# Kernel optimization log

Measured on AMD Instinct MI355X. Metric: run time of the kernel, lower is better.

Reference implementation:

```python
import jax, jax.numpy as jnp
import numpy as np


def _gcn_conv(x, edge_index, W, b):
    # PyG GCNConv: h = D^{-1/2} (A + I) D^{-1/2} (x @ W) + b
    n = x.shape[0]
    xw = x @ W  # [N, C]
    loop = jnp.arange(n, dtype=edge_index.dtype)
    row = jnp.concatenate([edge_index[0], loop])  # source (x_j)
    col = jnp.concatenate([edge_index[1], loop])  # target (aggregation index)
    deg = jax.ops.segment_sum(jnp.ones_like(col, dtype=xw.dtype), col, num_segments=n)
    dinv = jnp.where(deg > 0, deg ** -0.5, 0.0)
    norm = dinv[row] * dinv[col]  # [E+N]
    out = jax.ops.segment_sum(xw[row] * norm[:, None], col, num_segments=n)
    return out + b


def setup_inputs() -> dict:
    key = jax.random.key(0)
    ks = jax.random.split(key, 8)
    N, F, E = 100000, 512, 3200000
    W_SCALE = 0.1  # keep sigmoid un-saturated
    x = jax.random.normal(ks[0], (N, F), dtype=jnp.float32)
    edge_index = jax.random.randint(ks[1], (2, E), 0, N, dtype=jnp.int64)
    Wg = jax.random.normal(ks[2], (F, 16), dtype=jnp.float32) * W_SCALE
    bg = jnp.zeros((16,), dtype=jnp.float32)
    W1 = jax.random.normal(ks[3], (16, 16), dtype=jnp.float32) * W_SCALE
    b1 = jnp.zeros((16,), dtype=jnp.float32)
    W2 = jax.random.normal(ks[4], (16, 32), dtype=jnp.float32) * W_SCALE
    b2 = jnp.zeros((32,), dtype=jnp.float32)
    W3 = jax.random.normal(ks[5], (32, 1), dtype=jnp.float32) * W_SCALE
    b3 = jnp.zeros((1,), dtype=jnp.float32)
    return {"x": x, "edge_index": edge_index, "Wg": Wg, "bg": bg,
            "W1": W1, "b1": b1, "W2": W2, "b2": b2, "W3": W3, "b3": b3}


def reference(x, edge_index, Wg, bg, W1, b1, W2, b2, W3, b3):
    h = jax.nn.relu(_gcn_conv(x, edge_index, Wg, bg))
    h = jax.nn.relu(h @ W1 + b1)
    h = jax.nn.relu(h @ W2 + b2)
    return jax.nn.sigmoid(h @ W3 + b3)  # [N, 1]
```

## Files before the change

### kernel.cpp

```cpp
#include <hip/hip_runtime.h>
#include <math.h>


static constexpr int F = 512;
static constexpr int C = 16;
static constexpr int BSH = 7;
static constexpr int BSZ = 128;
static constexpr int NBMAX = 1024;
static constexpr int EPB = 16384;

__global__ __launch_bounds__(256) void k_xw_bcount(const float* __restrict__ x,
                                                   const float* __restrict__ Wg,
                                                   float* __restrict__ xw, int n,
                                                   const int* __restrict__ dst,
                                                   int* __restrict__ bh, int E, int gb)
{
    if ((int)blockIdx.x >= gb) {
        __shared__ int hist[NBMAX];
        for (int i = threadIdx.x; i < NBMAX; i += 256) hist[i] = 0;
        __syncthreads();
        int g = blockIdx.x - gb;
        int base = g * EPB;
#pragma unroll 4
        for (int j = 0; j < EPB / 256; ++j) {
            int e = base + j * 256 + threadIdx.x;
            if (e < E) atomicAdd(&hist[dst[e] >> BSH], 1);
        }
        __syncthreads();
        int* row = bh + (size_t)g * NBMAX;
        for (int i = threadIdx.x; i < NBMAX; i += 256) row[i] = hist[i];
        return;
    }
    int row = blockIdx.x * 256 + threadIdx.x;
    if (row >= n) return;
    float acc[C];
#pragma unroll
    for (int c = 0; c < C; ++c) acc[c] = 0.f;
    const float4* xr = (const float4*)(x + (size_t)row * F);
#pragma unroll 8
    for (int k4 = 0; k4 < F / 4; ++k4) {
        float4 xv = xr[k4];
        const float* w = Wg + k4 * 4 * C;
#pragma unroll
        for (int j = 0; j < 4; ++j) {
            float xs = (j == 0) ? xv.x : (j == 1) ? xv.y : (j == 2) ? xv.z : xv.w;
#pragma unroll
            for (int c = 0; c < C; ++c)
                acc[c] = fmaf(xs, w[j * C + c], acc[c]);
        }
    }
    float4* o = (float4*)(xw + (size_t)row * C);
#pragma unroll
    for (int q = 0; q < 4; ++q)
        o[q] = make_float4(acc[4 * q + 0], acc[4 * q + 1], acc[4 * q + 2], acc[4 * q + 3]);
}

__global__ __launch_bounds__(256) void k_bscatter(const int* __restrict__ ei,
                                                  const int* __restrict__ bh,
                                                  int* __restrict__ bstart,
                                                  int* __restrict__ packed,
                                                  int E, int geb)
{
    __shared__ int s_excl[NBMAX];
    __shared__ int cur[NBMAX];
    int g = blockIdx.x, t = threadIdx.x;

    int own[4], tot[4];
#pragma unroll
    for (int k = 0; k < 4; ++k) { own[k] = 0; tot[k] = 0; }
    int gg = 0;
    for (; gg + 4 <= geb; gg += 4) {
        int v[4][4];
#pragma unroll
        for (int j = 0; j < 4; ++j)
#pragma unroll
            for (int k = 0; k < 4; ++k)
                v[j][k] = bh[(size_t)(gg + j) * NBMAX + t + 256 * k];
#pragma unroll
        for (int j = 0; j < 4; ++j)
#pragma unroll
            for (int k = 0; k < 4; ++k) {
                if (gg + j == g) own[k] = tot[k];
                tot[k] += v[j][k];
            }
    }
    for (; gg < geb; ++gg) {
#pragma unroll
        for (int k = 0; k < 4; ++k) {
            int v = bh[(size_t)gg * NBMAX + t + 256 * k];
            if (gg == g) own[k] = tot[k];
            tot[k] += v;
        }
    }
#pragma unroll
    for (int k = 0; k < 4; ++k) s_excl[t + 256 * k] = tot[k];
    __syncthreads();

    int c0 = s_excl[4 * t], c1 = s_excl[4 * t + 1],
        c2 = s_excl[4 * t + 2], c3 = s_excl[4 * t + 3];
    int csum = c0 + c1 + c2 + c3;
    cur[t] = csum;
    __syncthreads();
    for (int d = 1; d < 256; d <<= 1) {
        int u = (t >= d) ? cur[t - d] : 0;
        __syncthreads();
        cur[t] += u;
        __syncthreads();
    }
    int chunk_excl = cur[t] - csum;
    __syncthreads();

    int e0 = chunk_excl, e1 = e0 + c0, e2 = e1 + c1, e3 = e2 + c2;
    s_excl[4 * t] = e0; s_excl[4 * t + 1] = e1;
    s_excl[4 * t + 2] = e2; s_excl[4 * t + 3] = e3;
    __syncthreads();

#pragma unroll
    for (int k = 0; k < 4; ++k)
        cur[t + 256 * k] = s_excl[t + 256 * k] + own[k];
    if (g == 0) {
#pragma unroll
        for (int k = 0; k < 4; ++k) bstart[t + 256 * k] = s_excl[t + 256 * k];
        if (t == 255) bstart[NBMAX] = e3 + c3;
    }
    __syncthreads();

    int base = g * EPB;
#pragma unroll 2
    for (int j = 0; j < EPB / 256; ++j) {
        int e = base + j * 256 + t;
        if (e < E) {
            int d = ei[E + e];
            int s = ei[e];
            int b = d >> BSH;
            int r = atomicAdd(&cur[b], 1);
            packed[r] = s | ((d & (BSZ - 1)) << 17);
        }
    }
}

__global__ __launch_bounds__(256) void k_bcsr(const int* __restrict__ packed,
                                              const int* __restrict__ bstart,
                                              float* __restrict__ y,
                                              int* __restrict__ srcs,
                                              int* __restrict__ starts,
                                              int* __restrict__ cnt,
                                              float* __restrict__ dinv, int n)
{
    int b = blockIdx.x, t = threadIdx.x;
    __shared__ int hist[BSZ];
    __shared__ int sc[BSZ];
    __shared__ float sdi[BSZ];
    if (t < BSZ) hist[t] = 0;
    __syncthreads();
    int beg = bstart[b], end = bstart[b + 1];
    for (int e = beg + t; e < end; e += 256)
        atomicAdd(&hist[(packed[e] >> 17) & (BSZ - 1)], 1);
    __syncthreads();
    int myc = 0;
    if (t < BSZ) { myc = hist[t]; sc[t] = myc; }
    __syncthreads();
    for (int d = 1; d < BSZ; d <<= 1) {
        int u = 0;
        if (t < BSZ && t >= d) u = sc[t - d];
        __syncthreads();
        if (t < BSZ) sc[t] += u;
        __syncthreads();
    }
    int node0 = b << BSH;
    if (t < BSZ) {
        int lst = sc[t] - myc;
        sc[t] = lst;
        float di = rsqrtf((float)(myc + 1));
        sdi[t] = di;
        int node = node0 + t;
        if (node < n) { starts[node] = beg + lst; cnt[node] = myc; dinv[node] = di; }
        hist[t] = 0;
    }
    __syncthreads();
    for (int e = beg + t; e < end; e += 256) {
        int p = packed[e];
        int dl = (p >> 17) & (BSZ - 1);
        int r = atomicAdd(&hist[dl], 1);
        srcs[beg + sc[dl] + r] = p & 0x1FFFF;
    }
    int nn = n - node0; if (nn > BSZ) nn = BSZ;
    if (nn <= 0) return;
    int lim = nn * 4;
    float4* yv = (float4*)(y + (size_t)node0 * C);
    for (int i = t; i < lim; i += 256) {
        float di = sdi[i >> 2];
        float4 v = yv[i];
        v.x *= di; v.y *= di; v.z *= di; v.w *= di;
        yv[i] = v;
    }
}

__global__ __launch_bounds__(256) void k_gather_mlp(const float* __restrict__ y,
                                                    const int* __restrict__ srcs,
                                                    const int* __restrict__ starts,
                                                    const int* __restrict__ cnt,
                                                    const float* __restrict__ dinv,
                                                    const float* __restrict__ bg,
                                                    const float* __restrict__ W1,
                                                    const float* __restrict__ b1,
                                                    const float* __restrict__ W2,
                                                    const float* __restrict__ b2,
                                                    const float* __restrict__ W3,
                                                    const float* __restrict__ b3,
                                                    float* __restrict__ out, int n)
{
    __shared__ float sh[64][17];
    int tid = threadIdx.x;
    int gtid = blockIdx.x * 256 + tid;
    int i = gtid >> 2;
    int q = tid & 3;
    if (i < n) {
        const float4* yv = (const float4*)y;
        float4 acc = yv[(size_t)i * 4 + q];
        int beg = starts[i];
        int end = beg + cnt[i];
        int e = beg;
        int headEnd = (beg + 3) & ~3;
        if (headEnd > end) headEnd = end;
        for (; e < headEnd; ++e) {
            float4 v = yv[(size_t)srcs[e] * 4 + q];
            acc.x += v.x; acc.y += v.y; acc.z += v.z; acc.w += v.w;
        }
        for (; e + 4 <= end; e += 4) {
            int4 s4 = *(const int4*)(srcs + e);
            float4 v0 = yv[(size_t)s4.x * 4 + q];
            float4 v1 = yv[(size_t)s4.y * 4 + q];
            float4 v2 = yv[(size_t)s4.z * 4 + q];
            float4 v3 = yv[(size_t)s4.w * 4 + q];
            acc.x += v0.x + v1.x + v2.x + v3.x;
            acc.y += v0.y + v1.y + v2.y + v3.y;
            acc.z += v0.z + v1.z + v2.z + v3.z;
            acc.w += v0.w + v1.w + v2.w + v3.w;
        }
        for (; e < end; ++e) {
            float4 v = yv[(size_t)srcs[e] * 4 + q];
            acc.x += v.x; acc.y += v.y; acc.z += v.z; acc.w += v.w;
        }
        float di = dinv[i];
        const float* bq = bg + q * 4;
        int lr = tid >> 2;
        sh[lr][4 * q + 0] = fmaxf(fmaf(acc.x, di, bq[0]), 0.f);
        sh[lr][4 * q + 1] = fmaxf(fmaf(acc.y, di, bq[1]), 0.f);
        sh[lr][4 * q + 2] = fmaxf(fmaf(acc.z, di, bq[2]), 0.f);
        sh[lr][4 * q + 3] = fmaxf(fmaf(acc.w, di, bq[3]), 0.f);
    }
    __syncthreads();
    if (tid < 64) {
        int node = blockIdx.x * 64 + tid;
        if (node < n) {
            float h[16];
#pragma unroll
            for (int k = 0; k < 16; ++k) h[k] = sh[tid][k];
            float h1[16];
#pragma unroll
            for (int c = 0; c < 16; ++c) {
                float s = b1[c];
#pragma unroll
                for (int k = 0; k < 16; ++k) s = fmaf(h[k], W1[k * 16 + c], s);
                h1[c] = fmaxf(s, 0.f);
            }
            float h2[32];
#pragma unroll
            for (int c = 0; c < 32; ++c) {
                float s = b2[c];
#pragma unroll
                for (int k = 0; k < 16; ++k) s = fmaf(h1[k], W2[k * 32 + c], s);
                h2[c] = fmaxf(s, 0.f);
            }
            float s = b3[0];
#pragma unroll
            for (int k = 0; k < 32; ++k) s = fmaf(h2[k], W3[k], s);
            out[node] = 1.f / (1.f + expf(-s));
        }
    }
}

extern "C" void kernel_launch(void* const* d_in, const int* in_sizes, int n_in,
                              void* d_out, int out_size, void* d_ws, size_t ws_size,
                              hipStream_t stream)
{
    const float* x  = (const float*)d_in[0];
    const int*   ei = (const int*)d_in[1];
    const float* Wg = (const float*)d_in[2];
    const float* bg = (const float*)d_in[3];
    const float* W1 = (const float*)d_in[4];
    const float* b1 = (const float*)d_in[5];
    const float* W2 = (const float*)d_in[6];
    const float* b2 = (const float*)d_in[7];
    const float* W3 = (const float*)d_in[8];
    const float* b3 = (const float*)d_in[9];
    float* out = (float*)d_out;

    int n = in_sizes[0] / F;
    int E = in_sizes[1] / 2;

    int gb  = (n + 255) / 256;
    int geb = (E + EPB - 1) / EPB;
    int NB  = (n + BSZ - 1) >> BSH;

    char* ws = (char*)d_ws;
    size_t off = 0;
    float* y      = (float*)(ws + off); off += (size_t)n * C * sizeof(float);
    int*   packed = (int*)  (ws + off); off += (size_t)E * sizeof(int);
    int*   srcs   = (int*)  (ws + off);
    int*   bh     = srcs;
    size_t big = (size_t)E; if ((size_t)geb * NBMAX > big) big = (size_t)geb * NBMAX;
    off += big * sizeof(int);
    int*   starts = (int*)  (ws + off); off += (size_t)((n + 3) & ~3) * sizeof(int);
    int*   cnt    = (int*)  (ws + off); off += (size_t)((n + 3) & ~3) * sizeof(int);
    float* dinv   = (float*)(ws + off); off += (size_t)((n + 3) & ~3) * sizeof(float);
    int*   bstart = (int*)  (ws + off);

    k_xw_bcount<<<gb + geb, 256, 0, stream>>>(x, Wg, y, n, ei + E, bh, E, gb);
    k_bscatter<<<geb, 256, 0, stream>>>(ei, bh, bstart, packed, E, geb);
    k_bcsr<<<NB, 256, 0, stream>>>(packed, bstart, y, srcs, starts, cnt, dinv, n);
    k_gather_mlp<<<(n + 63) / 64, 256, 0, stream>>>(y, srcs, starts, cnt, dinv, bg,
                                                    W1, b1, W2, b2, W3, b3, out, n);
}
```

Baseline: 484.9 us.

## Stage x tiles through padded shared memory with coalesced loads and register prefetch

The x@W GEMV kernel used to have each thread read its own 2KB row, so memory accesses were strided across lanes. It now loads 256x32 tiles with coalesced warp reads into a padded (33-stride) LDS buffer. The next chunk is prefetched into registers while the current one is being computed. This aims to improve DRAM coalescing for the 200MB read of x, at the cost of more LDS (about 33KB), extra syncs and 32 prefetch registers, which may lower occupancy.

Measured after the change: 594.2 us. +22.5%, slower.

```diff
diff --git a/kernel.cpp b/kernel.cpp
--- a/kernel.cpp
+++ b/kernel.cpp
@@ -15,8 +15,9 @@
                                                    const int* __restrict__ dst,
                                                    int* __restrict__ bh, int E, int gb)
 {
+    __shared__ float smem[256 * 33];
     if ((int)blockIdx.x >= gb) {
-        __shared__ int hist[NBMAX];
+        int* hist = (int*)smem;
         for (int i = threadIdx.x; i < NBMAX; i += 256) hist[i] = 0;
         __syncthreads();
         int g = blockIdx.x - gb;
@@ -31,28 +32,59 @@
         for (int i = threadIdx.x; i < NBMAX; i += 256) row[i] = hist[i];
         return;
     }
-    int row = blockIdx.x * 256 + threadIdx.x;
-    if (row >= n) return;
+    int t = threadIdx.x;
+    int row0 = blockIdx.x * 256;
+    int sr = t >> 5;
+    int sc = t & 31;
+
     float acc[C];
 #pragma unroll
     for (int c = 0; c < C; ++c) acc[c] = 0.f;
-    const float4* xr = (const float4*)(x + (size_t)row * F);
-#pragma unroll 8
-    for (int k4 = 0; k4 < F / 4; ++k4) {
-        float4 xv = xr[k4];
-        const float* w = Wg + k4 * 4 * C;
-#pragma unroll
-        for (int j = 0; j < 4; ++j) {
-            float xs = (j == 0) ? xv.x : (j == 1) ? xv.y : (j == 2) ? xv.z : xv.w;
+
+    float pf[32];
+#pragma unroll
+    for (int p = 0; p < 32; ++p) {
+        int r = sr + (p << 3);
+        int gr = row0 + r;
+        pf[p] = (gr < n) ? x[(size_t)gr * F + sc] : 0.f;
+    }
+#pragma unroll
+    for (int p = 0; p < 32; ++p) smem[(sr + (p << 3)) * 33 + sc] = pf[p];
+    __syncthreads();
+
+    for (int ch = 0; ch < 16; ++ch) {
+        if (ch < 15) {
+            int k0n = (ch + 1) * 32;
+#pragma unroll
+            for (int p = 0; p < 32; ++p) {
+                int r = sr + (p << 3);
+                int gr = row0 + r;
+                pf[p] = (gr < n) ? x[(size_t)gr * F + k0n + sc] : 0.f;
+            }
+        }
+        const float* wb = Wg + ch * 32 * C;
+        const float* ml = smem + t * 33;
+#pragma unroll
+        for (int kk = 0; kk < 32; ++kk) {
+            float xs = ml[kk];
 #pragma unroll
             for (int c = 0; c < C; ++c)
-                acc[c] = fmaf(xs, w[j * C + c], acc[c]);
-        }
-    }
-    float4* o = (float4*)(xw + (size_t)row * C);
-#pragma unroll
-    for (int q = 0; q < 4; ++q)
-        o[q] = make_float4(acc[4 * q + 0], acc[4 * q + 1], acc[4 * q + 2], acc[4 * q + 3]);
+                acc[c] = fmaf(xs, wb[kk * C + c], acc[c]);
+        }
+        __syncthreads();
+        if (ch < 15) {
+#pragma unroll
+            for (int p = 0; p < 32; ++p) smem[(sr + (p << 3)) * 33 + sc] = pf[p];
+            __syncthreads();
+        }
+    }
+    int myrow = row0 + t;
+    if (myrow < n) {
+        float4* o = (float4*)(xw + (size_t)myrow * C);
+#pragma unroll
+        for (int q = 0; q < 4; ++q)
+            o[q] = make_float4(acc[4 * q + 0], acc[4 * q + 1], acc[4 * q + 2], acc[4 * q + 3]);
+    }
 }
 
 __global__ __launch_bounds__(256) void k_bscatter(const int* __restrict__ ei,
```
